# Optimization experiments

Hardware: AMD Instinct MI355X
Metric: run time of the kernel (lower is better)

Reference implementation:

```python
import jax, jax.numpy as jnp
import numpy as np

B, N = 4, 512
C_IN = 64
HF = WF = 128
HO = WO = 512
HG = WG = 32            # patch grid size (Hi, Wi)
MAXR = 32.0
CTRL = 8                # ctrlpts = (8, 8)
NCTRL = CTRL * CTRL
NPARAM = NCTRL + 2
KFACTOR = 0.3
OFFSET = (1.0 - KFACTOR) / 2.0
BN_EPS = 1e-5


def bn_eval(t):
    # BatchNorm(affine=False) in eval mode with default running stats (mean=0, var=1)
    return t * (1.0 / np.sqrt(1.0 + BN_EPS)).astype(np.float32)


def conv2d(x, w, padding):
    return jax.lax.conv_general_dilated(
        x, w, (1, 1), padding, dimension_numbers=('NCHW', 'OIHW', 'NCHW'))


def bilinear_sample(img, ix, iy):
    # img [C,H,W]; ix, iy pixel coords of arbitrary shape S -> [C, *S]; zeros padding
    C, H, W = img.shape
    x0 = jnp.floor(ix); y0 = jnp.floor(iy)
    wx = ix - x0; wy = iy - y0

    def tap(xi, yi, w):
        valid = (xi >= 0) & (xi <= W - 1) & (yi >= 0) & (yi <= H - 1)
        xc = jnp.clip(xi, 0, W - 1).astype(jnp.int32)
        yc = jnp.clip(yi, 0, H - 1).astype(jnp.int32)
        return img[:, yc, xc] * (w * valid)[None]

    return (tap(x0, y0, (1 - wx) * (1 - wy)) + tap(x0 + 1, y0, wx * (1 - wy)) +
            tap(x0, y0 + 1, (1 - wx) * wy) + tap(x0 + 1, y0 + 1, wx * wy))


def coord_channels(x):
    b, c, h, w = x.shape
    gx = jnp.broadcast_to(jnp.linspace(-1.0, 1.0, w)[None, :], (h, w))
    gy = jnp.broadcast_to(jnp.linspace(-1.0, 1.0, h)[:, None], (h, w))
    coords = jnp.broadcast_to(jnp.stack([gx, gy])[None], (b, 2, h, w))
    return jnp.concatenate([x, coords.astype(x.dtype)], axis=1)


def get_polar_grid(kps, Hs, Ws):
    # kps [M,2] (x,y) pixel coords -> normalized sampling grid [M,HG,WG,2]
    xs = (jnp.arange(WG) + 0.5) * 2.0 / WG - 1.0   # affine_grid (align_corners=False)
    ys = (jnp.arange(HG) + 0.5) * 2.0 / HG - 1.0
    gx = jnp.broadcast_to(xs[None, :], (HG, WG)).reshape(-1)  # grid[...,0]
    gy = jnp.broadcast_to(ys[:, None], (HG, WG)).reshape(-1)  # grid[...,1]
    norm_g = (gx + 1.0) / 2.0
    r_ = 1.0 + norm_g * (MAXR - 1.0)               # 'linear' radial coords
    r_s = (r_ - 1.0) / (MAXR - 1.0) * 2.0 * MAXR / Ws
    t_s = (gy + 1.0) * np.pi
    xk = kps[:, 0:1] / Ws * 2.0 - 1.0
    yk = kps[:, 1:2] / Hs * 2.0 - 1.0
    aR = Ws / Hs
    x_s = r_s[None] * jnp.cos(t_s)[None] + xk
    y_s = r_s[None] * jnp.sin(t_s)[None] * aR + yk
    return jnp.stack([x_s, y_s], -1).reshape(-1, HG, WG, 2)


def tps(theta, ctrl, grid):
    # thin-plate spline surface: theta [M,T+2,2] (reduced), ctrl [M,T,2], grid [M,H,W,3]
    g = grid[..., 1:]
    r2 = jnp.maximum(
        (g ** 2).sum(-1)[..., None] + (ctrl ** 2).sum(-1)[:, None, None, :]
        - 2.0 * jnp.einsum('mhwk,mtk->mhwt', g, ctrl), 0.0)
    D = jnp.sqrt(r2 + 1e-12)
    U = r2 * jnp.log(D + 1e-6)                      # r^2 log r RBF
    w, a = theta[:, :-3, :], theta[:, -3:, :]
    w = jnp.concatenate([-w.sum(1, keepdims=True), w], axis=1)  # reduced (T+2) form
    b = jnp.einsum('mhwt,mtc->mhwc', U, w)
    z = jnp.einsum('mhwk,mkc->mhwc', grid, a)
    return z + b


def forward(x, in_imgs, keypts, conv1_w, conv2_w, lin1_w, lin1_b,
            lin2_w, lin2_b, lin3_w, lin3_b, Ho, Wo):
    Bn = x.shape[0]
    Nk = keypts.shape[1]
    # FCN with coordinate channels appended
    h = jax.nn.relu(bn_eval(conv2d(coord_channels(x), conv1_w, 'SAME')))
    Theta = jax.nn.relu(bn_eval(conv2d(h, conv2_w, 'VALID')))   # [B,2C,HF-2,WF-2]
    kps = keypts.astype(jnp.float32)                            # [B,N,2]
    Hf, Wf = Theta.shape[2], Theta.shape[3]

    # InterpolateSparse2d: bilinear sample of Theta at keypoints (align_corners=True)
    def interp_b(feat, pos):
        ix = pos[:, 0] / (Wo - 1) * (Wf - 1)
        iy = pos[:, 1] / (Ho - 1) * (Hf - 1)
        return bilinear_sample(feat, ix, iy).T                  # [N, 2C]

    th = jax.vmap(interp_b)(Theta, kps).reshape(Bn * Nk, -1)
    # attn MLP (eval mode: dropout off, BN1d with running stats)
    th = jax.nn.relu(bn_eval(th @ lin1_w.T + lin1_b))
    th = jax.nn.relu(th @ lin2_w.T + lin2_b)
    theta = jnp.tanh(th @ lin3_w.T + lin3_b).reshape(-1, NPARAM, 2)

    # per-keypoint polar grids, squeezed into [OFFSET, OFFSET+KFACTOR]
    pg = get_polar_grid(kps.reshape(-1, 2), float(Ho), float(Wo))  # [M,32,32,2]
    M = pg.shape[0]
    vmin = pg.reshape(M, -1, 2).min(1)[:, None, None, :]
    vmax = pg.reshape(M, -1, 2).max(1)[:, None, None, :]
    ptp = vmax - vmin
    pgn = (pg - vmin) / (ptp + 1e-8) * KFACTOR + OFFSET
    # F.interpolate(mode='nearest') 32x32 -> 8x8 control points: stride-4 subsample
    ctrl = pgn[:, ::HG // CTRL, ::WG // CTRL, :].reshape(M, -1, 2)
    Ipg = jnp.concatenate([jnp.ones(pgn.shape[:-1] + (1,), pgn.dtype), pgn], -1)
    warp = pgn + tps(theta, ctrl, Ipg)
    warp = ((warp - OFFSET) / KFACTOR) * ptp + vmin
    warp = warp.reshape(Bn, Nk, HG, WG, 2)

    # sample patches from input images (bilinear, align_corners=False, zeros padding)
    def sample_b(img, g):
        _, Hi, Wi = img.shape
        ix = ((g[..., 0] + 1.0) * Wi - 1.0) * 0.5
        iy = ((g[..., 1] + 1.0) * Hi - 1.0) * 0.5
        return jnp.transpose(bilinear_sample(img, ix, iy), (1, 0, 2, 3))  # [N,C,32,32]

    return jax.vmap(sample_b)(in_imgs, warp)  # [B,N,3,32,32]


def setup_inputs():
    key = jax.random.key(0)
    ks = jax.random.split(key, 8)
    return {
        'x': jax.random.normal(ks[0], (B, C_IN, HF, WF), jnp.float32),
        'in_imgs': jax.random.uniform(ks[1], (B, 3, HO, WO), jnp.float32),
        'keypts': jax.random.randint(ks[2], (B, N, 2), 0, HO).astype(jnp.int32),
        'conv1_w': jax.random.normal(ks[3], (2 * C_IN, C_IN + 2, 3, 3), jnp.float32) * 0.05,
        'conv2_w': jax.random.normal(ks[4], (2 * C_IN, 2 * C_IN, 3, 3), jnp.float32) * 0.05,
        'lin1_w': jax.random.normal(ks[5], (4 * C_IN, 2 * C_IN), jnp.float32) * 0.05,
        'lin1_b': jnp.zeros((4 * C_IN,), jnp.float32),
        'lin2_w': jax.random.normal(ks[6], (4 * C_IN, 4 * C_IN), jnp.float32) * 0.05,
        'lin2_b': jnp.zeros((4 * C_IN,), jnp.float32),
        'lin3_w': jax.random.normal(ks[7], (NPARAM * 2, 4 * C_IN), jnp.float32) * 1e-3,
        'lin3_b': jnp.zeros((NPARAM * 2,), jnp.float32),
        'Ho': HO,
        'Wo': WO,
    }


def reference(x, in_imgs, keypts, conv1_w, conv2_w, lin1_w, lin1_b,
              lin2_w, lin2_b, lin3_w, lin3_b, Ho, Wo):
    return forward(x, in_imgs, keypts, conv1_w, conv2_w, lin1_w, lin1_b,
                   lin2_w, lin2_b, lin3_w, lin3_b, Ho, Wo)
```

## Files before the change

### kernel.cpp

```cpp
#include <hip/hip_runtime.h>
#include <math.h>

#define MM 2048
#define HOImg 512
#define GG 1024
#define NCTRL 64
#define NPAR 132

#define BN_S 0.9999950000374997f

typedef __bf16 bf16x8 __attribute__((ext_vector_type(8)));
typedef float  f32x4  __attribute__((ext_vector_type(4)));

__device__ __forceinline__ unsigned short f2b(float v){
    unsigned u = __float_as_uint(v);
    unsigned r = (u + 0x7FFFu + ((u>>16)&1u)) >> 16;
    return (unsigned short)r;
}
__device__ __forceinline__ float b2f(unsigned short s){
    return __uint_as_float(((unsigned)s)<<16);
}

__global__ __launch_bounds__(256) void prep_xb_k(const float* __restrict__ x,
    short* __restrict__ XH)
{
    __shared__ float sT[64][65];
    const int xt = blockIdx.x, yo = blockIdx.y, b = blockIdx.z;
    const int tid = threadIdx.x;
    const int x0 = xt*64;

    if (yo == 0 || yo == 129){
        for (int e = tid; e < 4160; e += 256){
            int idx = xt*4160 + e;
            size_t o = (((size_t)b*130 + yo)*130 + idx/64)*64 + (idx&63);
            XH[o] = 0;
        }
        return;
    }
    const int ys = yo - 1;
    for (int e = tid; e < 64*64; e += 256) {
        int ci = e >> 6, xl = e & 63;
        sT[ci][xl] = x[(((size_t)b*64 + ci)*128 + ys)*128 + x0 + xl];
    }
    if (tid < 64){
        size_t o = (((size_t)b*130 + yo)*130 + (xt?129:0))*64 + tid;
        XH[o] = 0;
    }
    __syncthreads();
    for (int e = tid; e < 64*64; e += 256) {
        int xl = e >> 6, ci = e & 63;
        size_t o = (((size_t)b*130 + yo)*130 + (x0+xl+1))*64 + ci;
        XH[o] = (short)f2b(sT[ci][xl]);
    }
}

__global__ __launch_bounds__(256) void prep_misc_k(const float* __restrict__ w1,
    const float* __restrict__ w2, const float* __restrict__ l1w,
    const float* __restrict__ l2w, const float* __restrict__ l3w,
    short* __restrict__ B1H, short* __restrict__ B2H, float* __restrict__ Tab,
    unsigned short* __restrict__ W1h, unsigned short* __restrict__ W1l,
    unsigned short* __restrict__ W2h, unsigned short* __restrict__ W2l,
    unsigned short* __restrict__ W3h, unsigned short* __restrict__ W3l)
{
    int bid = blockIdx.x;
    if (bid < 128){
        int co = bid;
        for (int e = threadIdx.x; e < 576; e += 256){
            int kp = e >> 6, ci = e & 63;
            int ky = kp/3, kx = kp - (kp/3)*3;
            float v = w1[((co*66 + ci)*3 + ky)*3 + kx];
            B1H[co*576+e] = (short)f2b(v);
        }
    } else if (bid < 256){
        int co = bid - 128;
        for (int e = threadIdx.x; e < 1152; e += 256){
            int kp = e >> 7, ci = e & 127;
            int ky = kp/3, kx = kp - (kp/3)*3;
            float v = w2[((co*128 + ci)*3 + ky)*3 + kx];
            B2H[co*1152+e] = (short)f2b(v);
        }
    } else if (bid < 261){
        int i = (bid-256)*256 + threadIdx.x;
        if (i < 1152){
            int co = i/9, comb = i - (i/9)*9;
            int py = comb/3, px = comb - py*3;
            float w64[3][3], w65[3][3];
            #pragma unroll
            for (int ky=0;ky<3;ky++)
                #pragma unroll
                for (int kx=0;kx<3;kx++){
                    w64[ky][kx] = w1[((co*66 + 64)*3 + ky)*3 + kx];
                    w65[ky][kx] = w1[((co*66 + 65)*3 + ky)*3 + kx];
                }
            const int ky0 = (py==0)?1:0, ky1 = (py==2)?1:2;
            const int kx0 = (px==0)?1:0, kx1 = (px==2)?1:2;
            const float s = 2.f/127.f;
            float A = 0.f, Bc = 0.f, Cc = 0.f;
            for (int kx=kx0; kx<=kx1; ++kx){
                float wy = 0.f;
                for (int ky=ky0; ky<=ky1; ++ky) wy += w64[ky][kx];
                A  += wy * (-1.f + (float)(kx-1)*s);
                Bc += wy * s;
            }
            for (int ky=ky0; ky<=ky1; ++ky){
                float wx = 0.f;
                for (int kx=kx0; kx<=kx1; ++kx) wx += w65[ky][kx];
                A  += wx * (-1.f + (float)(ky-1)*s);
                Cc += wx * s;
            }
            float* d = Tab + ((size_t)comb*128 + co)*3;
            d[0] = A; d[1] = Bc; d[2] = Cc;
        }
    } else if (bid < 389){
        int e = (bid-261)*256 + threadIdx.x;
        float v = l1w[e];
        unsigned short hi = f2b(v);
        W1h[e] = hi; W1l[e] = f2b(v - b2f(hi));
    } else if (bid < 645){
        int e = (bid-389)*256 + threadIdx.x;
        float v = l2w[e];
        unsigned short hi = f2b(v);
        W2h[e] = hi; W2l[e] = f2b(v - b2f(hi));
    } else {
        int e = (bid-645)*256 + threadIdx.x;
        int o = e >> 8, k = e & 255;
        float v = (o < 132) ? l3w[o*256 + k] : 0.f;
        unsigned short hi = f2b(v);
        W3h[e] = hi; W3l[e] = f2b(v - b2f(hi));
    }
}

__global__ __launch_bounds__(256, 2) void spconv_k(
    const short* __restrict__ XP, const short* __restrict__ B1,
    const short* __restrict__ B2, const float* __restrict__ Tab,
    const int* __restrict__ kp, float* __restrict__ th0g)
{
    __shared__ __align__(16) short xL[10368];
    __shared__ __align__(16) short hL[8768];
    __shared__ int   sPY[4], sPX[4], sCY[4][2], sCX[4][2], sB[4];
    __shared__ float sWT[4][4];
    const int bid = blockIdx.x;
    const int tid = threadIdx.x;
    const int wv = tid>>6, lane = tid&63;
    const int l15 = lane&15, lg = lane>>4;

    if (tid < 4){
        int m = bid*4 + tid;
        sB[tid] = m >> 9;
        float ix = (float)kp[m*2+0]/511.f*125.f;
        float iy = (float)kp[m*2+1]/511.f*125.f;
        float x0f = floorf(ix), y0f = floorf(iy);
        float wx = ix-x0f, wy = iy-y0f;
        int X0 = (int)x0f, Y0 = (int)y0f;
        bool vx1 = (x0f+1.f <= 125.f), vy1 = (y0f+1.f <= 125.f);
        int X1 = vx1 ? X0+1 : 125;
        int Y1 = vy1 ? Y0+1 : 125;
        int pX0 = min(X0,124), pY0 = min(Y0,124);
        sPX[tid]=pX0; sPY[tid]=pY0;
        sCX[tid][0]=X0-pX0; sCX[tid][1]=X1-pX0;
        sCY[tid][0]=Y0-pY0; sCY[tid][1]=Y1-pY0;
        sWT[tid][0] = (1.f-wx)*(1.f-wy);
        sWT[tid][1] = vx1 ? wx*(1.f-wy) : 0.f;
        sWT[tid][2] = vy1 ? (1.f-wx)*wy : 0.f;
        sWT[tid][3] = (vx1&&vy1) ? wx*wy : 0.f;
    }
    __syncthreads();

    for (int e = tid; e < 1152; e += 256){
        int pair = e >> 3, seg = e & 7;
        int ki = pair/36, rem = pair - ki*36;
        int row = rem/6, col = rem - row*6;
        const short* src = XP + (((size_t)sB[ki]*130 + sPY[ki]+row)*130
                                 + sPX[ki]+col)*64 + seg*8;
        int4 v = *(const int4*)src;
        *(int4*)&xL[(ki*36 + rem)*72 + seg*8] = v;
    }
    __syncthreads();

    f32x4 a1[4][2];
    #pragma unroll
    for (int i=0;i<4;i++){ a1[i][0]=(f32x4)(0.f); a1[i][1]=(f32x4)(0.f); }
    {
        const int py = l15>>2, px = l15&3;
        for (int cc=0; cc<2; ++cc){
            #pragma unroll
            for (int k9=0;k9<9;k9++){
                const int ky = k9/3, kx = k9 - (k9/3)*3;
                bf16x8 A[4], Bv[2];
                #pragma unroll
                for (int mt=0;mt<4;mt++)
                    A[mt] = *(const bf16x8*)&xL[(mt*36 + (py+ky)*6 + (px+kx))*72
                                                + cc*32 + lg*8];
                const int ko = k9*64 + cc*32;
                Bv[0] = *(const bf16x8*)(B1 + (wv*32 +     l15)*576 + ko + lg*8);
                Bv[1] = *(const bf16x8*)(B1 + (wv*32 + 16 + l15)*576 + ko + lg*8);
                #pragma unroll
                for (int mt=0;mt<4;mt++){
                    a1[mt][0] = __builtin_amdgcn_mfma_f32_16x16x32_bf16(A[mt], Bv[0], a1[mt][0],0,0,0);
                    a1[mt][1] = __builtin_amdgcn_mfma_f32_16x16x32_bf16(A[mt], Bv[1], a1[mt][1],0,0,0);
                }
            }
        }
    }
    #pragma unroll
    for (int mt=0;mt<4;mt++){
        const int pY0 = sPY[mt], pX0 = sPX[mt];
        #pragma unroll
        for (int reg=0;reg<4;reg++){
            const int p = lg*4 + reg;
            const int py = p>>2, px = p&3;
            const int hy = pY0+py, hx = pX0+px;
            const int pyb = (hy==0)?0:((hy==127)?2:1);
            const int pxb = (hx==0)?0:((hx==127)?2:1);
            #pragma unroll
            for (int nt=0;nt<2;nt++){
                const int co = wv*32 + nt*16 + l15;
                const float* t3 = Tab + ((size_t)(pyb*3+pxb)*128 + co)*3;
                float a = a1[mt][nt][reg];
                a += t3[0] + t3[1]*(float)hx + t3[2]*(float)hy;
                float v = fmaxf(a*BN_S, 0.f);
                hL[mt*2192 + p*136 + co] = (short)f2b(v);
            }
        }
    }
    __syncthreads();

    f32x4 a2[2];
    a2[0]=(f32x4)(0.f); a2[1]=(f32x4)(0.f);
    {
        const int ki = l15>>2, c = l15&3, cy = c>>1, cx = c&1;
        const int hbase = ki*2192 + (sCY[ki][cy]*4 + sCX[ki][cx])*136;
        for (int cc=0; cc<4; ++cc){
            #pragma unroll
            for (int k9=0;k9<9;k9++){
                const int ky = k9/3, kx = k9 - (k9/3)*3;
                bf16x8 A = *(const bf16x8*)&hL[hbase + (ky*4+kx)*136 + cc*32 + lg*8];
                const int ko = k9*128 + cc*32;
                bf16x8 Bv0 = *(const bf16x8*)(B2 + (wv*32 +     l15)*1152 + ko + lg*8);
                bf16x8 Bv1 = *(const bf16x8*)(B2 + (wv*32 + 16 + l15)*1152 + ko + lg*8);
                a2[0] = __builtin_amdgcn_mfma_f32_16x16x32_bf16(A, Bv0, a2[0],0,0,0);
                a2[1] = __builtin_amdgcn_mfma_f32_16x16x32_bf16(A, Bv1, a2[1],0,0,0);
            }
        }
    }
    {
        const float* w4 = sWT[lg];
        #pragma unroll
        for (int nt=0;nt<2;nt++){
            float c0 = fmaxf(a2[nt][0]*BN_S, 0.f);
            float c1 = fmaxf(a2[nt][1]*BN_S, 0.f);
            float c2 = fmaxf(a2[nt][2]*BN_S, 0.f);
            float c3 = fmaxf(a2[nt][3]*BN_S, 0.f);
            float r = ((c0*w4[0] + c1*w4[1]) + c2*w4[2]) + c3*w4[3];
            th0g[(size_t)(bid*4+lg)*128 + wv*32 + nt*16 + l15] = r;
        }
    }
}

__global__ __launch_bounds__(1024) void consts_red_k(float* __restrict__ cbuf,
    float* __restrict__ pgn, float* __restrict__ ctrl)
{
    __shared__ float part[16][4];
    __shared__ float res[4];
    int g = threadIdx.x;
    int i = g >> 5, j = g & 31;
    float xs = (j + 0.5f)*(2.0f/32.0f) - 1.0f;
    float ys = (i + 0.5f)*(2.0f/32.0f) - 1.0f;
    float norm = (xs + 1.0f)*0.5f;
    float r_ = 1.0f + norm*31.0f;
    float r_s = (r_ - 1.0f)/31.0f*2.0f*32.0f/512.0f;
    float t_s = (ys + 1.0f)*3.14159265358979323846f;
    float bx = r_s*cosf(t_s);
    float by = r_s*sinf(t_s);

    float mnx=bx, mxx=bx, mny=by, mxy=by;
    #pragma unroll
    for (int s=1; s<64; s<<=1){
        mnx = fminf(mnx, __shfl_xor(mnx, s));
        mxx = fmaxf(mxx, __shfl_xor(mxx, s));
        mny = fminf(mny, __shfl_xor(mny, s));
        mxy = fmaxf(mxy, __shfl_xor(mxy, s));
    }
    int wv = g>>6, ln = g&63;
    if (ln == 0){ part[wv][0]=mnx; part[wv][1]=mxx; part[wv][2]=mny; part[wv][3]=mxy; }
    __syncthreads();
    if (g < 4){
        float v = part[0][g];
        for (int t=1;t<16;t++) v = (g&1) ? fmaxf(v, part[t][g]) : fminf(v, part[t][g]);
        res[g] = v;
    }
    __syncthreads();
    float minx=res[0], maxx=res[1], miny=res[2], maxy=res[3];
    float ptpx = maxx-minx, ptpy = maxy-miny;
    if (g == 0){ cbuf[0]=minx; cbuf[1]=miny; cbuf[2]=ptpx; cbuf[3]=ptpy; }

    float pgx = (bx - minx)/(ptpx + 1e-8f)*0.3f + 0.35f;
    float pgy = (by - miny)/(ptpy + 1e-8f)*0.3f + 0.35f;
    pgn[2*g]   = pgx;
    pgn[2*g+1] = pgy;
    if ((i&3)==0 && (j&3)==0){ int t = (i>>2)*8 + (j>>2); ctrl[t*2]=pgx; ctrl[t*2+1]=pgy; }
}

__global__ __launch_bounds__(256) void ug_fill_k(const float* __restrict__ pgn,
    const float* __restrict__ ctrl, unsigned short* __restrict__ Ug)
{
    __shared__ float sc[64][2];
    int g = blockIdx.x*256 + threadIdx.x;
    for (int e = threadIdx.x; e < 128; e += 256) sc[e>>1][e&1] = ctrl[e];
    __syncthreads();
    float px = pgn[2*g], py = pgn[2*g+1];
    float gg2 = px*px + py*py;
    unsigned int* dst = (unsigned int*)(Ug + (size_t)g*96);
    #pragma unroll
    for (int t=0;t<64;t+=2){
        float cx0=sc[t][0],   cy0=sc[t][1];
        float cx1=sc[t+1][0], cy1=sc[t+1][1];
        float r20 = fmaxf(gg2 + (cx0*cx0+cy0*cy0) - 2.f*(px*cx0+py*cy0), 0.f);
        float r21 = fmaxf(gg2 + (cx1*cx1+cy1*cy1) - 2.f*(px*cx1+py*cy1), 0.f);
        float u0 = r20*logf(sqrtf(r20+1e-12f)+1e-6f);
        float u1 = r21*logf(sqrtf(r21+1e-12f)+1e-6f);
        dst[t>>1] = (unsigned)f2b(u0) | ((unsigned)f2b(u1)<<16);
    }
    dst[32] = (unsigned)f2b(1.f) | ((unsigned)f2b(px)<<16);
    dst[33] = (unsigned)f2b(py);
    #pragma unroll
    for (int t=34;t<48;t++) dst[t] = 0u;
}

__global__ __launch_bounds__(256) void mlp_tps_k(const float* __restrict__ th0g,
    const unsigned short* __restrict__ W1h, const unsigned short* __restrict__ W1l,
    const unsigned short* __restrict__ W2h, const unsigned short* __restrict__ W2l,
    const unsigned short* __restrict__ W3h, const unsigned short* __restrict__ W3l,
    const float* __restrict__ l1b, const float* __restrict__ l2b,
    const float* __restrict__ l3b,
    const unsigned short* __restrict__ Ug, float* __restrict__ bxy)
{
    __shared__ unsigned short th0h[16][136], th0l[16][136];
    __shared__ unsigned short th1h[16][264], th1l[16][264];
    __shared__ unsigned short th2h[16][264], th2l[16][264];
    __shared__ float sth[8][132];
    __shared__ __align__(16) unsigned short sW[16][96];
    const int m0 = blockIdx.x*8;
    const int tid = threadIdx.x;
    const int wv = tid>>6, lane = tid&63;
    const int l15 = lane&15, lg = lane>>4;

    for (int e = tid; e < 2048; e += 256){
        int r = e >> 7, k = e & 127;
        float v = (r < 8) ? th0g[(size_t)(m0 + r)*128 + k] : 0.f;
        unsigned short hi = f2b(v);
        th0h[r][k] = hi; th0l[r][k] = f2b(v - b2f(hi));
    }
    __syncthreads();

    {
        f32x4 acc[4];
        #pragma unroll
        for (int nt=0;nt<4;nt++) acc[nt] = (f32x4)(0.f);
        for (int kc=0; kc<4; ++kc){
            bf16x8 Ah = *(const bf16x8*)&th0h[l15][kc*32 + lg*8];
            bf16x8 Al = *(const bf16x8*)&th0l[l15][kc*32 + lg*8];
            #pragma unroll
            for (int nt=0;nt<4;nt++){
                const int o = (wv*4+nt)*16 + l15;
                bf16x8 Bh = *(const bf16x8*)(W1h + (size_t)o*128 + kc*32 + lg*8);
                bf16x8 Bl = *(const bf16x8*)(W1l + (size_t)o*128 + kc*32 + lg*8);
                acc[nt] = __builtin_amdgcn_mfma_f32_16x16x32_bf16(Ah, Bh, acc[nt],0,0,0);
                acc[nt] = __builtin_amdgcn_mfma_f32_16x16x32_bf16(Ah, Bl, acc[nt],0,0,0);
                acc[nt] = __builtin_amdgcn_mfma_f32_16x16x32_bf16(Al, Bh, acc[nt],0,0,0);
            }
        }
        #pragma unroll
        for (int nt=0;nt<4;nt++){
            const int o = (wv*4+nt)*16 + l15;
            float bv = l1b[o];
            #pragma unroll
            for (int reg=0;reg<4;reg++){
                int r = lg*4+reg;
                float v = fmaxf((acc[nt][reg]+bv)*BN_S, 0.f);
                unsigned short hi = f2b(v);
                th1h[r][o] = hi; th1l[r][o] = f2b(v - b2f(hi));
            }
        }
    }
    __syncthreads();

    {
        f32x4 acc[4];
        #pragma unroll
        for (int nt=0;nt<4;nt++) acc[nt] = (f32x4)(0.f);
        for (int kc=0; kc<8; ++kc){
            bf16x8 Ah = *(const bf16x8*)&th1h[l15][kc*32 + lg*8];
            bf16x8 Al = *(const bf16x8*)&th1l[l15][kc*32 + lg*8];
            #pragma unroll
            for (int nt=0;nt<4;nt++){
                const int o = (wv*4+nt)*16 + l15;
                bf16x8 Bh = *(const bf16x8*)(W2h + (size_t)o*256 + kc*32 + lg*8);
                bf16x8 Bl = *(const bf16x8*)(W2l + (size_t)o*256 + kc*32 + lg*8);
                acc[nt] = __builtin_amdgcn_mfma_f32_16x16x32_bf16(Ah, Bh, acc[nt],0,0,0);
                acc[nt] = __builtin_amdgcn_mfma_f32_16x16x32_bf16(Ah, Bl, acc[nt],0,0,0);
                acc[nt] = __builtin_amdgcn_mfma_f32_16x16x32_bf16(Al, Bh, acc[nt],0,0,0);
            }
        }
        #pragma unroll
        for (int nt=0;nt<4;nt++){
            const int o = (wv*4+nt)*16 + l15;
            float bv = l2b[o];
            #pragma unroll
            for (int reg=0;reg<4;reg++){
                int r = lg*4+reg;
                float v = fmaxf(acc[nt][reg]+bv, 0.f);
                unsigned short hi = f2b(v);
                th2h[r][o] = hi; th2l[r][o] = f2b(v - b2f(hi));
            }
        }
    }
    __syncthreads();

    {
        f32x4 acc[3];
        #pragma unroll
        for (int t=0;t<3;t++) acc[t] = (f32x4)(0.f);
        const int nfr = (wv<3) ? 2 : 3;
        for (int kc=0; kc<8; ++kc){
            bf16x8 Ah = *(const bf16x8*)&th2h[l15][kc*32 + lg*8];
            bf16x8 Al = *(const bf16x8*)&th2l[l15][kc*32 + lg*8];
            for (int t=0;t<3;t++){
                if (t >= nfr) break;
                const int fr = (wv<3) ? (wv*2+t) : (6+t);
                const int o = fr*16 + l15;
                bf16x8 Bh = *(const bf16x8*)(W3h + (size_t)o*256 + kc*32 + lg*8);
                bf16x8 Bl = *(const bf16x8*)(W3l + (size_t)o*256 + kc*32 + lg*8);
                acc[t] = __builtin_amdgcn_mfma_f32_16x16x32_bf16(Ah, Bh, acc[t],0,0,0);
                acc[t] = __builtin_amdgcn_mfma_f32_16x16x32_bf16(Ah, Bl, acc[t],0,0,0);
                acc[t] = __builtin_amdgcn_mfma_f32_16x16x32_bf16(Al, Bh, acc[t],0,0,0);
            }
        }
        for (int t=0;t<3;t++){
            if (t >= nfr) break;
            const int fr = (wv<3) ? (wv*2+t) : (6+t);
            const int o = fr*16 + l15;
            if (o < NPAR){
                float bv = l3b[o];
                #pragma unroll
                for (int reg=0;reg<4;reg++){
                    int r = lg*4+reg;
                    if (r < 8) sth[r][o] = tanhf(acc[t][reg]+bv);
                }
            }
        }
    }
    __syncthreads();

    if (tid < 16){
        int kpi = tid>>1, c = tid&1;
        float s = 0.f;
        for (int p=0;p<63;p++){ float w = sth[kpi][2*p+c]; s += w; sW[tid][1+p] = f2b(w); }
        sW[tid][0]  = f2b(-s);
        sW[tid][64] = f2b(sth[kpi][126+c]);
        sW[tid][65] = f2b(sth[kpi][128+c]);
        sW[tid][66] = f2b(sth[kpi][130+c]);
        for (int p=67;p<96;p++) sW[tid][p] = 0;
    }
    __syncthreads();
    bf16x8 Bf[3];
    #pragma unroll
    for (int ks=0;ks<3;ks++) Bf[ks] = *(const bf16x8*)&sW[l15][ks*32 + lg*8];
    const int gbase = wv*256;
    const int kpg = m0 + (l15>>1), c = l15&1;
    #pragma unroll
    for (int mf=0; mf<16; ++mf){
        f32x4 acc2 = (f32x4)(0.f);
        const unsigned short* ap = Ug + (size_t)(gbase + mf*16 + l15)*96 + lg*8;
        #pragma unroll
        for (int ks=0;ks<3;ks++){
            bf16x8 Af = *(const bf16x8*)(ap + ks*32);
            acc2 = __builtin_amdgcn_mfma_f32_16x16x32_bf16(Af, Bf[ks], acc2,0,0,0);
        }
        float* dst = bxy + ((size_t)kpg*2 + c)*1024 + gbase + mf*16 + lg*4;
        #pragma unroll
        for (int r=0;r<4;r++) dst[r] = acc2[r];
    }
}

__global__ __launch_bounds__(256) void sample3_k(const int* __restrict__ kp,
    const float* __restrict__ bxy, const float* __restrict__ pgn,
    const float* __restrict__ cbuf, const float* __restrict__ imgs,
    float* __restrict__ out)
{
    const int bid = blockIdx.x;
    const int m = ((bid & 7) << 8) | (bid >> 3);
    const int ch = blockIdx.y;
    const int tid = threadIdx.x;
    const int b = m >> 9;
    const float vminx = cbuf[0] + ((float)kp[m*2+0]/512.f*2.f - 1.f);
    const float vminy = cbuf[1] + ((float)kp[m*2+1]/512.f*2.f - 1.f);
    const float ptpx = cbuf[2], ptpy = cbuf[3];
    const int g0 = tid*4;
    f32x4 zbx = *(const f32x4*)&bxy[((size_t)m*2+0)*1024 + g0];
    f32x4 zby = *(const f32x4*)&bxy[((size_t)m*2+1)*1024 + g0];
    f32x4 pga = *(const f32x4*)&pgn[2*g0];
    f32x4 pgb = *(const f32x4*)&pgn[2*g0+4];
    float px[4] = {pga[0], pga[2], pgb[0], pgb[2]};
    float py[4] = {pga[1], pga[3], pgb[1], pgb[3]};
    const float* ic = imgs + ((size_t)b*3 + ch)*HOImg*HOImg;
    f32x4 o;
    #pragma unroll
    for (int i=0;i<4;i++){
        float wnx = px[i] + zbx[i];
        float wny = py[i] + zby[i];
        float wxr = (wnx - 0.35f)/0.3f*ptpx + vminx;
        float wyr = (wny - 0.35f)/0.3f*ptpy + vminy;
        float ix = ((wxr + 1.f)*512.f - 1.f)*0.5f;
        float iy = ((wyr + 1.f)*512.f - 1.f)*0.5f;
        float x0f = floorf(ix), y0f = floorf(iy);
        float fx = ix-x0f, fy = iy-y0f;
        float w00=(1.f-fx)*(1.f-fy), w10=fx*(1.f-fy), w01=(1.f-fx)*fy, w11=fx*fy;
        bool vx0 = (x0f>=0.f)&&(x0f<=511.f), vx1 = (x0f+1.f>=0.f)&&(x0f+1.f<=511.f);
        bool vy0 = (y0f>=0.f)&&(y0f<=511.f), vy1 = (y0f+1.f>=0.f)&&(y0f+1.f<=511.f);
        float m00 = (vx0&&vy0)?w00:0.f;
        float m10 = (vx1&&vy0)?w10:0.f;
        float m01 = (vx0&&vy1)?w01:0.f;
        float m11 = (vx1&&vy1)?w11:0.f;
        int X0 = (int)fminf(fmaxf(x0f,0.f),511.f);
        int X1 = (int)fminf(fmaxf(x0f+1.f,0.f),511.f);
        int Y0 = (int)fminf(fmaxf(y0f,0.f),511.f);
        int Y1 = (int)fminf(fmaxf(y0f+1.f,0.f),511.f);
        int i00 = Y0*HOImg+X0, i10 = Y0*HOImg+X1, i01 = Y1*HOImg+X0, i11 = Y1*HOImg+X1;
        o[i] = ic[i00]*m00 + ic[i10]*m10 + ic[i01]*m01 + ic[i11]*m11;
    }
    *(f32x4*)&out[((size_t)(m*3+ch))*GG + g0] = o;
}

extern "C" void kernel_launch(void* const* d_in, const int* in_sizes, int n_in,
                              void* d_out, int out_size, void* d_ws, size_t ws_size,
                              hipStream_t stream)
{
    const float* x    = (const float*)d_in[0];
    const float* imgs = (const float*)d_in[1];
    const int*   kp   = (const int*)d_in[2];
    const float* c1w  = (const float*)d_in[3];
    const float* c2w  = (const float*)d_in[4];
    const float* l1w  = (const float*)d_in[5];
    const float* l1b  = (const float*)d_in[6];
    const float* l2w  = (const float*)d_in[7];
    const float* l2b  = (const float*)d_in[8];
    const float* l3w  = (const float*)d_in[9];
    const float* l3b  = (const float*)d_in[10];
    float* out = (float*)d_out;

    char* W = (char*)d_ws;
    short* xph   = (short*)(W + 0);
    constexpr size_t OFF_HH = 32514048;
    float* th0g = (float*)(W + OFF_HH);
    constexpr size_t OFF_B = OFF_HH + 17039360;
    short* B1 = (short*)(W + OFF_B);
    short* B2 = (short*)(W + OFF_B + 221184);
    constexpr size_t OFF_C = OFF_B + 516096;
    unsigned short* Ug  = (unsigned short*)(W + OFF_C);
    float* pgn  = (float*)(W + OFF_C + 196608);
    float* cbuf = (float*)(W + OFF_C + 204800);
    float* ctrl = (float*)(W + OFF_C + 205056);
    float* Tab  = (float*)(W + OFF_C + 205568);
    unsigned short* W1h = (unsigned short*)(W + OFF_C + 219392);
    unsigned short* W1l = (unsigned short*)(W + OFF_C + 284928);
    unsigned short* W2h = (unsigned short*)(W + OFF_C + 350464);
    unsigned short* W2l = (unsigned short*)(W + OFF_C + 481536);
    unsigned short* W3h = (unsigned short*)(W + OFF_C + 612608);
    unsigned short* W3l = (unsigned short*)(W + OFF_C + 686336);
    float* bxy = (float*)(W + OFF_C + 760064);

    hipLaunchKernelGGL(prep_xb_k, dim3(2,130,4), dim3(256), 0, stream, x, xph);
    hipLaunchKernelGGL(prep_misc_k, dim3(789), dim3(256), 0, stream,
                       c1w, c2w, l1w, l2w, l3w, B1, B2, Tab,
                       W1h, W1l, W2h, W2l, W3h, W3l);
    hipLaunchKernelGGL(consts_red_k, dim3(1), dim3(1024), 0, stream, cbuf, pgn, ctrl);
    hipLaunchKernelGGL(ug_fill_k, dim3(4), dim3(256), 0, stream, pgn, ctrl, Ug);

    hipLaunchKernelGGL(spconv_k, dim3(MM/4), dim3(256), 0, stream,
                       xph, B1, B2, Tab, kp, th0g);

    hipLaunchKernelGGL(mlp_tps_k, dim3(MM/8), dim3(256), 0, stream,
                       th0g, W1h, W1l, W2h, W2l, W3h, W3l,
                       l1b, l2b, l3b, Ug, bxy);
    hipLaunchKernelGGL(sample3_k, dim3(MM, 3), dim3(256), 0, stream,
                       kp, bxy, pgn, cbuf, imgs, out);
}
```

Baseline: 120.9 us.

## Interleave image channels for single-gather sampling and fuse constants into ug_fill

Adds a prep kernel that transposes the input images into an interleaved 4-float-per-pixel layout so the bilinear sampler fetches all three channels with one vector load per tap and runs in a single launch instead of one per channel. The polar-grid min/max reduction kernel is merged into ug_fill, with each block recomputing the reduction and control points, removing a launch and a global round-trip. The cost is an extra full pass over the images and 33% wasted bandwidth from the padding channel.

```diff
diff --git a/kernel.cpp b/kernel.cpp
--- a/kernel.cpp
+++ b/kernel.cpp
@@ -52,6 +52,20 @@
         size_t o = (((size_t)b*130 + yo)*130 + (x0+xl+1))*64 + ci;
         XH[o] = (short)f2b(sT[ci][xl]);
     }
+}
+
+__global__ __launch_bounds__(256) void prep_img_k(const float* __restrict__ imgs,
+    float* __restrict__ imgT)
+{
+    const int x = blockIdx.x*256 + threadIdx.x;
+    const int y = blockIdx.y, b = blockIdx.z;
+    const size_t ib = ((size_t)b*3*HOImg + y)*HOImg + x;
+    f32x4 v;
+    v[0] = imgs[ib];
+    v[1] = imgs[ib + (size_t)HOImg*HOImg];
+    v[2] = imgs[ib + (size_t)2*HOImg*HOImg];
+    v[3] = 0.f;
+    *(f32x4*)&imgT[(((size_t)b*HOImg + y)*HOImg + x)*4] = v;
 }
 
 __global__ __launch_bounds__(256) void prep_misc_k(const float* __restrict__ w1,
@@ -257,23 +271,33 @@
     }
 }
 
-__global__ __launch_bounds__(1024) void consts_red_k(float* __restrict__ cbuf,
-    float* __restrict__ pgn, float* __restrict__ ctrl)
-{
-    __shared__ float part[16][4];
+__global__ __launch_bounds__(256) void ug_fill_k(float* __restrict__ cbuf,
+    float* __restrict__ pgn, unsigned short* __restrict__ Ug)
+{
+    __shared__ float part[4][4];
     __shared__ float res[4];
-    int g = threadIdx.x;
-    int i = g >> 5, j = g & 31;
-    float xs = (j + 0.5f)*(2.0f/32.0f) - 1.0f;
-    float ys = (i + 0.5f)*(2.0f/32.0f) - 1.0f;
-    float norm = (xs + 1.0f)*0.5f;
-    float r_ = 1.0f + norm*31.0f;
-    float r_s = (r_ - 1.0f)/31.0f*2.0f*32.0f/512.0f;
-    float t_s = (ys + 1.0f)*3.14159265358979323846f;
-    float bx = r_s*cosf(t_s);
-    float by = r_s*sinf(t_s);
-
-    float mnx=bx, mxx=bx, mny=by, mxy=by;
+    __shared__ float sc[64][2];
+    const int tid = threadIdx.x;
+    const int bid = blockIdx.x;
+
+    float bxv[4], byv[4];
+    float mnx=1e30f, mxx=-1e30f, mny=1e30f, mxy=-1e30f;
+    #pragma unroll
+    for (int t=0;t<4;t++){
+        int g = tid + t*256;
+        int i = g >> 5, j = g & 31;
+        float xs = (j + 0.5f)*(2.0f/32.0f) - 1.0f;
+        float ys = (i + 0.5f)*(2.0f/32.0f) - 1.0f;
+        float norm = (xs + 1.0f)*0.5f;
+        float r_ = 1.0f + norm*31.0f;
+        float r_s = (r_ - 1.0f)/31.0f*2.0f*32.0f/512.0f;
+        float t_s = (ys + 1.0f)*3.14159265358979323846f;
+        float bx = r_s*cosf(t_s);
+        float by = r_s*sinf(t_s);
+        bxv[t]=bx; byv[t]=by;
+        mnx=fminf(mnx,bx); mxx=fmaxf(mxx,bx);
+        mny=fminf(mny,by); mxy=fmaxf(mxy,by);
+    }
     #pragma unroll
     for (int s=1; s<64; s<<=1){
         mnx = fminf(mnx, __shfl_xor(mnx, s));
@@ -281,34 +305,46 @@
         mny = fminf(mny, __shfl_xor(mny, s));
         mxy = fmaxf(mxy, __shfl_xor(mxy, s));
     }
-    int wv = g>>6, ln = g&63;
+    int wv = tid>>6, ln = tid&63;
     if (ln == 0){ part[wv][0]=mnx; part[wv][1]=mxx; part[wv][2]=mny; part[wv][3]=mxy; }
     __syncthreads();
-    if (g < 4){
-        float v = part[0][g];
-        for (int t=1;t<16;t++) v = (g&1) ? fmaxf(v, part[t][g]) : fminf(v, part[t][g]);
-        res[g] = v;
-    }
-    __syncthreads();
-    float minx=res[0], maxx=res[1], miny=res[2], maxy=res[3];
-    float ptpx = maxx-minx, ptpy = maxy-miny;
-    if (g == 0){ cbuf[0]=minx; cbuf[1]=miny; cbuf[2]=ptpx; cbuf[3]=ptpy; }
-
-    float pgx = (bx - minx)/(ptpx + 1e-8f)*0.3f + 0.35f;
-    float pgy = (by - miny)/(ptpy + 1e-8f)*0.3f + 0.35f;
-    pgn[2*g]   = pgx;
-    pgn[2*g+1] = pgy;
-    if ((i&3)==0 && (j&3)==0){ int t = (i>>2)*8 + (j>>2); ctrl[t*2]=pgx; ctrl[t*2+1]=pgy; }
-}
-
-__global__ __launch_bounds__(256) void ug_fill_k(const float* __restrict__ pgn,
-    const float* __restrict__ ctrl, unsigned short* __restrict__ Ug)
-{
-    __shared__ float sc[64][2];
-    int g = blockIdx.x*256 + threadIdx.x;
-    for (int e = threadIdx.x; e < 128; e += 256) sc[e>>1][e&1] = ctrl[e];
-    __syncthreads();
-    float px = pgn[2*g], py = pgn[2*g+1];
+    if (tid < 4){
+        float v = part[0][tid];
+        for (int t=1;t<4;t++) v = (tid&1) ? fmaxf(v, part[t][tid]) : fminf(v, part[t][tid]);
+        res[tid] = v;
+    }
+    __syncthreads();
+    const float minx=res[0], maxx=res[1], miny=res[2], maxy=res[3];
+    const float ptpx = maxx-minx, ptpy = maxy-miny;
+    if (bid == 0 && tid == 0){ cbuf[0]=minx; cbuf[1]=miny; cbuf[2]=ptpx; cbuf[3]=ptpy; }
+
+    #pragma unroll
+    for (int t=0;t<4;t++){
+        int g = tid + t*256;
+        float pgx = (bxv[t] - minx)/(ptpx + 1e-8f)*0.3f + 0.35f;
+        float pgy = (byv[t] - miny)/(ptpy + 1e-8f)*0.3f + 0.35f;
+        pgn[2*g]   = pgx;
+        pgn[2*g+1] = pgy;
+    }
+    if (tid < 64){
+        int g = 128*(tid>>3) + 4*(tid&7);
+        int i = g >> 5, j = g & 31;
+        float xs = (j + 0.5f)*(2.0f/32.0f) - 1.0f;
+        float ys = (i + 0.5f)*(2.0f/32.0f) - 1.0f;
+        float norm = (xs + 1.0f)*0.5f;
+        float r_ = 1.0f + norm*31.0f;
+        float r_s = (r_ - 1.0f)/31.0f*2.0f*32.0f/512.0f;
+        float t_s = (ys + 1.0f)*3.14159265358979323846f;
+        float bx = r_s*cosf(t_s);
+        float by = r_s*sinf(t_s);
+        sc[tid][0] = (bx - minx)/(ptpx + 1e-8f)*0.3f + 0.35f;
+        sc[tid][1] = (by - miny)/(ptpy + 1e-8f)*0.3f + 0.35f;
+    }
+    __syncthreads();
+
+    const float px = (bxv[bid] - minx)/(ptpx + 1e-8f)*0.3f + 0.35f;
+    const float py = (byv[bid] - miny)/(ptpy + 1e-8f)*0.3f + 0.35f;
+    const int g = bid*256 + tid;
     float gg2 = px*px + py*py;
     unsigned int* dst = (unsigned int*)(Ug + (size_t)g*96);
     #pragma unroll
@@ -483,14 +519,13 @@
     }
 }
 
-__global__ __launch_bounds__(256) void sample3_k(const int* __restrict__ kp,
+__global__ __launch_bounds__(256) void sample_k(const int* __restrict__ kp,
     const float* __restrict__ bxy, const float* __restrict__ pgn,
-    const float* __restrict__ cbuf, const float* __restrict__ imgs,
+    const float* __restrict__ cbuf, const float* __restrict__ imgT,
     float* __restrict__ out)
 {
     const int bid = blockIdx.x;
     const int m = ((bid & 7) << 8) | (bid >> 3);
-    const int ch = blockIdx.y;
     const int tid = threadIdx.x;
     const int b = m >> 9;
     const float vminx = cbuf[0] + ((float)kp[m*2+0]/512.f*2.f - 1.f);
@@ -503,8 +538,8 @@
     f32x4 pgb = *(const f32x4*)&pgn[2*g0+4];
     float px[4] = {pga[0], pga[2], pgb[0], pgb[2]};
     float py[4] = {pga[1], pga[3], pgb[1], pgb[3]};
-    const float* ic = imgs + ((size_t)b*3 + ch)*HOImg*HOImg;
-    f32x4 o;
+    const float* it_b = imgT + (size_t)b*HOImg*HOImg*4;
+    f32x4 o0, o1, o2;
     #pragma unroll
     for (int i=0;i<4;i++){
         float wnx = px[i] + zbx[i];
@@ -526,10 +561,17 @@
         int X1 = (int)fminf(fmaxf(x0f+1.f,0.f),511.f);
         int Y0 = (int)fminf(fmaxf(y0f,0.f),511.f);
         int Y1 = (int)fminf(fmaxf(y0f+1.f,0.f),511.f);
-        int i00 = Y0*HOImg+X0, i10 = Y0*HOImg+X1, i01 = Y1*HOImg+X0, i11 = Y1*HOImg+X1;
-        o[i] = ic[i00]*m00 + ic[i10]*m10 + ic[i01]*m01 + ic[i11]*m11;
-    }
-    *(f32x4*)&out[((size_t)(m*3+ch))*GG + g0] = o;
+        f32x4 t00 = *(const f32x4*)&it_b[((size_t)Y0*HOImg + X0)*4];
+        f32x4 t10 = *(const f32x4*)&it_b[((size_t)Y0*HOImg + X1)*4];
+        f32x4 t01 = *(const f32x4*)&it_b[((size_t)Y1*HOImg + X0)*4];
+        f32x4 t11 = *(const f32x4*)&it_b[((size_t)Y1*HOImg + X1)*4];
+        o0[i] = t00[0]*m00 + t10[0]*m10 + t01[0]*m01 + t11[0]*m11;
+        o1[i] = t00[1]*m00 + t10[1]*m10 + t01[1]*m01 + t11[1]*m11;
+        o2[i] = t00[2]*m00 + t10[2]*m10 + t01[2]*m01 + t11[2]*m11;
+    }
+    *(f32x4*)&out[((size_t)(m*3+0))*GG + g0] = o0;
+    *(f32x4*)&out[((size_t)(m*3+1))*GG + g0] = o1;
+    *(f32x4*)&out[((size_t)(m*3+2))*GG + g0] = o2;
 }
 
 extern "C" void kernel_launch(void* const* d_in, const int* in_sizes, int n_in,
@@ -550,32 +592,29 @@
     float* out = (float*)d_out;
 
     char* W = (char*)d_ws;
-    short* xph   = (short*)(W + 0);
-    constexpr size_t OFF_HH = 32514048;
-    float* th0g = (float*)(W + OFF_HH);
-    constexpr size_t OFF_B = OFF_HH + 17039360;
-    short* B1 = (short*)(W + OFF_B);
-    short* B2 = (short*)(W + OFF_B + 221184);
-    constexpr size_t OFF_C = OFF_B + 516096;
-    unsigned short* Ug  = (unsigned short*)(W + OFF_C);
-    float* pgn  = (float*)(W + OFF_C + 196608);
-    float* cbuf = (float*)(W + OFF_C + 204800);
-    float* ctrl = (float*)(W + OFF_C + 205056);
-    float* Tab  = (float*)(W + OFF_C + 205568);
-    unsigned short* W1h = (unsigned short*)(W + OFF_C + 219392);
-    unsigned short* W1l = (unsigned short*)(W + OFF_C + 284928);
-    unsigned short* W2h = (unsigned short*)(W + OFF_C + 350464);
-    unsigned short* W2l = (unsigned short*)(W + OFF_C + 481536);
-    unsigned short* W3h = (unsigned short*)(W + OFF_C + 612608);
-    unsigned short* W3l = (unsigned short*)(W + OFF_C + 686336);
-    float* bxy = (float*)(W + OFF_C + 760064);
+    short* xph  = (short*)(W + 0);
+    float* imgT = (float*)(W + 8652800);
+    float* th0g = (float*)(W + 25430016);
+    short* B1   = (short*)(W + 26478592);
+    short* B2   = (short*)(W + 26626048);
+    float* Tab  = (float*)(W + 26920960);
+    unsigned short* Ug  = (unsigned short*)(W + 26934784);
+    float* pgn  = (float*)(W + 27131392);
+    float* cbuf = (float*)(W + 27139584);
+    unsigned short* W1h = (unsigned short*)(W + 27140352);
+    unsigned short* W1l = (unsigned short*)(W + 27205888);
+    unsigned short* W2h = (unsigned short*)(W + 27271424);
+    unsigned short* W2l = (unsigned short*)(W + 27402496);
+    unsigned short* W3h = (unsigned short*)(W + 27533568);
+    unsigned short* W3l = (unsigned short*)(W + 27607296);
+    float* bxy  = (float*)(W + 27681024);
 
     hipLaunchKernelGGL(prep_xb_k, dim3(2,130,4), dim3(256), 0, stream, x, xph);
+    hipLaunchKernelGGL(prep_img_k, dim3(2,512,4), dim3(256), 0, stream, imgs, imgT);
     hipLaunchKernelGGL(prep_misc_k, dim3(789), dim3(256), 0, stream,
                        c1w, c2w, l1w, l2w, l3w, B1, B2, Tab,
                        W1h, W1l, W2h, W2l, W3h, W3l);
-    hipLaunchKernelGGL(consts_red_k, dim3(1), dim3(1024), 0, stream, cbuf, pgn, ctrl);
-    hipLaunchKernelGGL(ug_fill_k, dim3(4), dim3(256), 0, stream, pgn, ctrl, Ug);
+    hipLaunchKernelGGL(ug_fill_k, dim3(4), dim3(256), 0, stream, cbuf, pgn, Ug);
 
     hipLaunchKernelGGL(spconv_k, dim3(MM/4), dim3(256), 0, stream,
                        xph, B1, B2, Tab, kp, th0g);
@@ -583,6 +622,6 @@
     hipLaunchKernelGGL(mlp_tps_k, dim3(MM/8), dim3(256), 0, stream,
                        th0g, W1h, W1l, W2h, W2l, W3h, W3l,
                        l1b, l2b, l3b, Ug, bxy);
-    hipLaunchKernelGGL(sample3_k, dim3(MM, 3), dim3(256), 0, stream,
-                       kp, bxy, pgn, cbuf, imgs, out);
-}
+    hipLaunchKernelGGL(sample_k, dim3(MM), dim3(256), 0, stream,
+                       kp, bxy, pgn, cbuf, imgT, out);
+}
```

Result: no change. 119.7 us (-1.0%).
